# Optimization experiments

Hardware: AMD Instinct MI355X
Metric: run time of the kernel (lower is better)

The kernel has to match this reference:

```python
import jax, jax.numpy as jnp
import numpy as np

D_MODEL = 256
D_AUDIO = 256
W2V_DIM = 768
LIB_DIM = 93
N_LAYERS = 4
D_STATE = 16
D_CONV = 4
EXPAND = 2
D_INNER = EXPAND * D_MODEL  # 512
DT_RANK = (D_MODEL + 15) // 16  # 16
B, L = 8, 1024


def _silu(x):
    return x * jax.nn.sigmoid(x)


def _layernorm(x, g, b):
    mu = jnp.mean(x, axis=-1, keepdims=True)
    var = jnp.mean((x - mu) ** 2, axis=-1, keepdims=True)
    return (x - mu) * jax.lax.rsqrt(var + 1e-5) * g + b


def _mamba(x, in_W, conv_W, conv_b, xproj_W, dt_W, dt_b, A_log, D_vec, out_W):
    # x: [B, L, d_model]
    xz = jnp.einsum('bld,ed->ble', x, in_W)          # [B, L, 2*d_inner]
    xc, z = jnp.split(xz, 2, axis=-1)
    # causal depthwise conv1d over time
    u = jnp.swapaxes(xc, 1, 2)                        # [B, d_inner, L]
    u = jax.lax.conv_general_dilated(
        u, conv_W[:, None, :], (1,), [(D_CONV - 1, 0)],
        dimension_numbers=('NCH', 'OIH', 'NCH'), feature_group_count=D_INNER)
    xc = _silu(jnp.swapaxes(u, 1, 2) + conv_b)        # [B, L, d_inner]
    dbl = jnp.einsum('bld,ed->ble', xc, xproj_W)      # [B, L, dt_rank+2*d_state]
    dt, Bm, Cm = jnp.split(dbl, [DT_RANK, DT_RANK + D_STATE], axis=-1)
    dt = jax.nn.softplus(jnp.einsum('blr,dr->bld', dt, dt_W) + dt_b)  # [B, L, d_inner]
    A = -jnp.exp(A_log)                               # [d_inner, d_state]

    def step(h, inp):
        dt_t, x_t, B_t, C_t = inp                     # [B,d_inner],[B,d_inner],[B,S],[B,S]
        dA = jnp.exp(dt_t[..., None] * A)             # [B, d_inner, S]
        h = h * dA + (dt_t * x_t)[..., None] * B_t[:, None, :]
        y = jnp.einsum('bds,bs->bd', h, C_t)
        return h, y

    h0 = jnp.zeros((x.shape[0], D_INNER, D_STATE), x.dtype)
    xs = (jnp.swapaxes(dt, 0, 1), jnp.swapaxes(xc, 0, 1),
          jnp.swapaxes(Bm, 0, 1), jnp.swapaxes(Cm, 0, 1))
    _, ys = jax.lax.scan(step, h0, xs)                # ys: [L, B, d_inner]
    y = jnp.swapaxes(ys, 0, 1) + xc * D_vec
    y = y * _silu(z)
    return jnp.einsum('bld,ed->ble', y, out_W)


def setup_inputs() -> dict:
    key = jax.random.key(0)
    ks = jax.random.split(key, 24)

    def g(k, shape, scale):
        return (jax.random.normal(k, shape, dtype=jnp.float32) * scale)

    inp = {}
    inp['wav2vec_feat'] = jax.random.normal(ks[0], (B, L, W2V_DIM), dtype=jnp.float32)
    inp['librosa_feat'] = jax.random.normal(ks[1], (B, L, LIB_DIM), dtype=jnp.float32)
    inp['w2v_W'] = g(ks[2], (D_AUDIO, W2V_DIM), W2V_DIM ** -0.5)
    inp['w2v_b'] = jnp.zeros((D_AUDIO,), jnp.float32)
    inp['lib_W'] = g(ks[3], (D_AUDIO, LIB_DIM), LIB_DIM ** -0.5)
    inp['lib_b'] = jnp.zeros((D_AUDIO,), jnp.float32)
    inp['fuse_W'] = g(ks[4], (D_MODEL, 2 * D_AUDIO), (2 * D_AUDIO) ** -0.5)
    inp['fuse_b'] = jnp.zeros((D_MODEL,), jnp.float32)
    inp['proj_W'] = g(ks[5], (D_MODEL, D_MODEL), D_MODEL ** -0.5)
    inp['proj_b'] = jnp.zeros((D_MODEL,), jnp.float32)
    # stacked per-layer Mamba params, leading dim = N_LAYERS
    inp['ln_g'] = jnp.ones((N_LAYERS, D_MODEL), jnp.float32)
    inp['ln_b'] = jnp.zeros((N_LAYERS, D_MODEL), jnp.float32)
    inp['in_W'] = g(ks[6], (N_LAYERS, 2 * D_INNER, D_MODEL), D_MODEL ** -0.5)
    inp['conv_W'] = g(ks[7], (N_LAYERS, D_INNER, D_CONV), D_CONV ** -0.5)
    inp['conv_b'] = jnp.zeros((N_LAYERS, D_INNER), jnp.float32)
    inp['xproj_W'] = g(ks[8], (N_LAYERS, DT_RANK + 2 * D_STATE, D_INNER), D_INNER ** -0.5)
    inp['dt_W'] = g(ks[9], (N_LAYERS, D_INNER, DT_RANK), DT_RANK ** -0.5)
    inp['dt_b'] = jnp.full((N_LAYERS, D_INNER), -4.6, jnp.float32)  # softplus -> ~0.01
    A0 = jnp.log(jnp.arange(1, D_STATE + 1, dtype=jnp.float32))
    inp['A_log'] = jnp.broadcast_to(A0, (N_LAYERS, D_INNER, D_STATE)).copy()
    inp['D_vec'] = jnp.ones((N_LAYERS, D_INNER), jnp.float32)
    inp['out_W'] = g(ks[10], (N_LAYERS, D_MODEL, D_INNER), D_INNER ** -0.5)
    inp['fnorm_g'] = jnp.ones((D_MODEL,), jnp.float32)
    inp['fnorm_b'] = jnp.zeros((D_MODEL,), jnp.float32)
    return inp


def reference(wav2vec_feat, librosa_feat, w2v_W, w2v_b, lib_W, lib_b,
              fuse_W, fuse_b, proj_W, proj_b, ln_g, ln_b, in_W, conv_W, conv_b,
              xproj_W, dt_W, dt_b, A_log, D_vec, out_W, fnorm_g, fnorm_b):
    w = jnp.einsum('bld,ed->ble', wav2vec_feat, w2v_W) + w2v_b
    l = jnp.einsum('bld,ed->ble', librosa_feat, lib_W) + lib_b
    h = jnp.einsum('bld,ed->ble', jnp.concatenate([w, l], axis=-1), fuse_W) + fuse_b
    # MambaEncoder: proj -> blocks -> final norm
    h = jnp.einsum('bld,ed->ble', h, proj_W) + proj_b
    for i in range(N_LAYERS):
        h = h + _mamba(_layernorm(h, ln_g[i], ln_b[i]), in_W[i], conv_W[i],
                       conv_b[i], xproj_W[i], dt_W[i], dt_b[i], A_log[i],
                       D_vec[i], out_W[i])
    return _layernorm(h, fnorm_g, fnorm_b)
```

## Files before the change

### kernel.cpp

```cpp
#include <hip/hip_runtime.h>
#include <math.h>


#define CH 64
#define CT 16

typedef __attribute__((ext_vector_type(8))) short bfrag8;
typedef __attribute__((ext_vector_type(4))) float floatx4;

__device__ __forceinline__ float silu_f(float x) { return x / (1.f + __expf(-x)); }
__device__ __forceinline__ unsigned short f2bf(float x) {
    union { float f; unsigned int u; } c; c.f = x;
    unsigned int r = (c.u + 0x7fffu + ((c.u >> 16) & 1u)) >> 16;
    return (unsigned short)r;
}
__device__ __forceinline__ float bf2f(unsigned short u) {
    union { unsigned int u; float f; } c; c.u = ((unsigned int)u) << 16; return c.f;
}
__device__ __forceinline__ floatx4 exp4(floatx4 x) {
    floatx4 r;
    r[0] = __expf(x[0]); r[1] = __expf(x[1]); r[2] = __expf(x[2]); r[3] = __expf(x[3]);
    return r;
}

#define NJOBS 6
struct CvtJobs {
    const float* src[NJOBS];
    unsigned short* dst[NJOBS];
    int n_tot[NJOBS];
    int start_blk[NJOBS + 1];
};
__global__ void conv_bf16_multi(CvtJobs J)
{
    int blk = blockIdx.x;
    int job = 0;
    while (job + 1 < NJOBS && blk >= J.start_blk[job + 1]) job++;
    int i = (blk - J.start_blk[job]) * 1024 + threadIdx.x * 4;
    if (i >= J.n_tot[job]) return;
    const float* src = J.src[job];
    unsigned short* dst = J.dst[job];
    float4 v = *(const float4*)(src + i);
    dst[i] = f2bf(v.x); dst[i+1] = f2bf(v.y); dst[i+2] = f2bf(v.z); dst[i+3] = f2bf(v.w);
}

__global__ void pad_bf16_kernel(const float* __restrict__ src, unsigned short* __restrict__ dst,
                                int rows, int cs, int cd)
{
    int i = blockIdx.x * 256 + threadIdx.x;
    if (i >= rows * cd) return;
    int row = i / cd, c = i - row * cd;
    dst[i] = (c < cs) ? f2bf(src[row * cs + c]) : (unsigned short)0;
}

template<int RM, int RN>
__global__ __launch_bounds__(64)
void dmfma_gemm(const unsigned short* __restrict__ A, int lda,
                const unsigned short* __restrict__ W, int ldw,
                int K, const float* __restrict__ bias, const float* __restrict__ Cin,
                float* __restrict__ Cf32, unsigned short* __restrict__ Cbf16,
                int N, int ldc, int act)
{
    int lane = threadIdx.x;
    int lm = lane & 15, qk = lane >> 4;
    int m0 = blockIdx.y * (16 * RM);
    int n0 = blockIdx.x * (16 * RN);

    const unsigned short* Ab = A + (size_t)(m0 + lm) * lda + qk * 8;
    const unsigned short* Wb = W + (size_t)(n0 + lm) * ldw + qk * 8;

    floatx4 acc[RM][RN];
#pragma unroll
    for (int i = 0; i < RM; i++)
#pragma unroll
        for (int j = 0; j < RN; j++) acc[i][j] = (floatx4){0.f, 0.f, 0.f, 0.f};

    bfrag8 af[RM], wf[RN];
#pragma unroll
    for (int i = 0; i < RM; i++) af[i] = *(const bfrag8*)(Ab + (size_t)i * 16 * lda);
#pragma unroll
    for (int j = 0; j < RN; j++) wf[j] = *(const bfrag8*)(Wb + (size_t)j * 16 * ldw);

    for (int k0 = 32; k0 < K; k0 += 32) {
        bfrag8 afn[RM], wfn[RN];
#pragma unroll
        for (int i = 0; i < RM; i++) afn[i] = *(const bfrag8*)(Ab + (size_t)i * 16 * lda + k0);
#pragma unroll
        for (int j = 0; j < RN; j++) wfn[j] = *(const bfrag8*)(Wb + (size_t)j * 16 * ldw + k0);
#pragma unroll
        for (int i = 0; i < RM; i++)
#pragma unroll
            for (int j = 0; j < RN; j++)
                acc[i][j] = __builtin_amdgcn_mfma_f32_16x16x32_bf16(af[i], wf[j], acc[i][j], 0, 0, 0);
#pragma unroll
        for (int i = 0; i < RM; i++) af[i] = afn[i];
#pragma unroll
        for (int j = 0; j < RN; j++) wf[j] = wfn[j];
    }
#pragma unroll
    for (int i = 0; i < RM; i++)
#pragma unroll
        for (int j = 0; j < RN; j++)
            acc[i][j] = __builtin_amdgcn_mfma_f32_16x16x32_bf16(af[i], wf[j], acc[i][j], 0, 0, 0);

#pragma unroll
    for (int i = 0; i < RM; i++) {
        int mrow = m0 + i * 16 + qk * 4;
#pragma unroll
        for (int j = 0; j < RN; j++) {
            int n = n0 + j * 16 + lm;
            if (n < N) {
#pragma unroll
                for (int r = 0; r < 4; r++) {
                    float v = acc[i][j][r];
                    size_t o = (size_t)(mrow + r) * ldc + n;
                    if (bias) v += bias[n];
                    if (act == 1) v = fmaxf(v, 0.f) + log1pf(__expf(-fabsf(v)));
                    if (Cin) v += Cin[o];
                    if (Cf32) Cf32[o] = v;
                    if (Cbf16) Cbf16[o] = f2bf(v);
                }
            }
        }
    }
}

__global__ void ln_kernel(const float* __restrict__ x, const float* __restrict__ g,
                          const float* __restrict__ b, float* __restrict__ yf,
                          unsigned short* __restrict__ ybf)
{
    int row = blockIdx.x * 4 + (threadIdx.x >> 6);
    int lane = threadIdx.x & 63;
    size_t o = (size_t)row * 256 + lane * 4;
    floatx4 v = *(const floatx4*)(x + o);
    float s1 = v[0] + v[1] + v[2] + v[3];
    float s2 = v[0]*v[0] + v[1]*v[1] + v[2]*v[2] + v[3]*v[3];
#pragma unroll
    for (int off = 1; off < 64; off <<= 1) {
        s1 += __shfl_xor(s1, off);
        s2 += __shfl_xor(s2, off);
    }
    float mu = s1 * (1.f / 256.f);
    float var = s2 * (1.f / 256.f) - mu * mu;
    float rs = rsqrtf(var + 1e-5f);
    floatx4 gv = *(const floatx4*)(g + lane * 4);
    floatx4 bv = *(const floatx4*)(b + lane * 4);
    floatx4 out = (v - mu) * rs * gv + bv;
    if (yf) *(floatx4*)(yf + o) = out;
    if (ybf) {
        ushort4 pk;
        pk.x = f2bf(out[0]); pk.y = f2bf(out[1]); pk.z = f2bf(out[2]); pk.w = f2bf(out[3]);
        *(ushort4*)(ybf + o) = pk;
    }
}

__global__ void conv_silu_kernel(const unsigned short* __restrict__ xz, const float* __restrict__ cw,
                                 const float* __restrict__ cb, unsigned short* __restrict__ xc)
{
    int idx = blockIdx.x * 256 + threadIdx.x;
    int d4 = (idx & 127) << 2;
    int bt = idx >> 7;
    int t = bt & 1023;
    floatx4 acc = *(const floatx4*)(cb + d4);
    floatx4 w0 = *(const floatx4*)(cw + d4 * 4);
    floatx4 w1 = *(const floatx4*)(cw + d4 * 4 + 4);
    floatx4 w2 = *(const floatx4*)(cw + d4 * 4 + 8);
    floatx4 w3 = *(const floatx4*)(cw + d4 * 4 + 12);
#pragma unroll
    for (int j = 0; j < 4; j++) {
        int tt = t + j - 3;
        if (tt >= 0) {
            ushort4 v = *(const ushort4*)(xz + (size_t)(bt + j - 3) * 1024 + d4);
            acc[0] += bf2f(v.x) * w0[j];
            acc[1] += bf2f(v.y) * w1[j];
            acc[2] += bf2f(v.z) * w2[j];
            acc[3] += bf2f(v.w) * w3[j];
        }
    }
    ushort4 o;
    o.x = f2bf(silu_f(acc[0])); o.y = f2bf(silu_f(acc[1]));
    o.z = f2bf(silu_f(acc[2])); o.w = f2bf(silu_f(acc[3]));
    *(ushort4*)(xc + (size_t)bt * 512 + d4) = o;
}

__global__ __launch_bounds__(256, 4)
void scan_local_kernel(const unsigned short* __restrict__ xc, const float* __restrict__ dbl,
                       const unsigned short* __restrict__ dtb, const float* __restrict__ A_log,
                       const float* __restrict__ Dvec,
                       float* __restrict__ dtsums, float* __restrict__ Hbuf,
                       float* __restrict__ ypart)
{
    int bi = blockIdx.x;
    int dgrp = bi & 1;
    int chunk = (bi >> 1) & (CH - 1);
    int b = bi >> 7;
    int d = dgrp * 256 + threadIdx.x;

    floatx4 a0 = -exp4(*(const floatx4*)(A_log + d * 16));
    floatx4 a1 = -exp4(*(const floatx4*)(A_log + d * 16 + 4));
    floatx4 a2 = -exp4(*(const floatx4*)(A_log + d * 16 + 8));
    floatx4 a3 = -exp4(*(const floatx4*)(A_log + d * 16 + 12));
    float dcoef = Dvec[d];

    floatx4 z4 = (floatx4){0.f, 0.f, 0.f, 0.f};
    floatx4 h0 = z4, h1 = z4, h2 = z4, h3 = z4;
    float dtsum = 0.f;

    size_t rbt = (size_t)b * 1024 + chunk * CT;
    float dt_v = bf2f(dtb[rbt * 512 + d]);
    float x_v  = bf2f(xc[rbt * 512 + d]);
    const float* row = dbl + rbt * 48;
    floatx4 B0 = *(const floatx4*)(row + 16);
    floatx4 B1 = *(const floatx4*)(row + 20);
    floatx4 B2 = *(const floatx4*)(row + 24);
    floatx4 B3 = *(const floatx4*)(row + 28);

    for (int t = 0; t < CT - 1; t++) {
        size_t r2 = rbt + 1;
        float dt_n = bf2f(dtb[r2 * 512 + d]);
        float x_n  = bf2f(xc[r2 * 512 + d]);
        const float* rown = dbl + r2 * 48;
        floatx4 Bn0 = *(const floatx4*)(rown + 16);
        floatx4 Bn1 = *(const floatx4*)(rown + 20);
        floatx4 Bn2 = *(const floatx4*)(rown + 24);
        floatx4 Bn3 = *(const floatx4*)(rown + 28);

        float dtx = dt_v * x_v;
        dtsum += dt_v;
        floatx4 dA;
        dA = exp4(dt_v * a0); h0 = h0 * dA + dtx * B0;
        dA = exp4(dt_v * a1); h1 = h1 * dA + dtx * B1;
        dA = exp4(dt_v * a2); h2 = h2 * dA + dtx * B2;
        dA = exp4(dt_v * a3); h3 = h3 * dA + dtx * B3;
        floatx4 C0 = *(const floatx4*)(row + 32);
        floatx4 C1 = *(const floatx4*)(row + 36);
        floatx4 C2 = *(const floatx4*)(row + 40);
        floatx4 C3 = *(const floatx4*)(row + 44);
        floatx4 yv = h0 * C0 + h1 * C1 + h2 * C2 + h3 * C3;
        ypart[rbt * 512 + d] = yv[0] + yv[1] + yv[2] + yv[3] + x_v * dcoef;

        dt_v = dt_n; x_v = x_n;
        B0 = Bn0; B1 = Bn1; B2 = Bn2; B3 = Bn3;
        row = rown; rbt = r2;
    }
    {
        float dtx = dt_v * x_v;
        dtsum += dt_v;
        floatx4 dA;
        dA = exp4(dt_v * a0); h0 = h0 * dA + dtx * B0;
        dA = exp4(dt_v * a1); h1 = h1 * dA + dtx * B1;
        dA = exp4(dt_v * a2); h2 = h2 * dA + dtx * B2;
        dA = exp4(dt_v * a3); h3 = h3 * dA + dtx * B3;
        floatx4 C0 = *(const floatx4*)(row + 32);
        floatx4 C1 = *(const floatx4*)(row + 36);
        floatx4 C2 = *(const floatx4*)(row + 40);
        floatx4 C3 = *(const floatx4*)(row + 44);
        floatx4 yv = h0 * C0 + h1 * C1 + h2 * C2 + h3 * C3;
        ypart[rbt * 512 + d] = yv[0] + yv[1] + yv[2] + yv[3] + x_v * dcoef;
    }
    size_t base = (size_t)chunk * 65536 + ((b * 512 + d) * 16);
    *(floatx4*)&Hbuf[base]      = h0;
    *(floatx4*)&Hbuf[base + 4]  = h1;
    *(floatx4*)&Hbuf[base + 8]  = h2;
    *(floatx4*)&Hbuf[base + 12] = h3;
    dtsums[chunk * 4096 + b * 512 + d] = dtsum;
}

__global__ void scan_carry_kernel(const float* __restrict__ dtsums, const float* __restrict__ A_log,
                                  float* __restrict__ Hbuf)
{
    int ch = blockIdx.x * 256 + threadIdx.x;
    int s = ch & 15;
    int bd = ch >> 4;
    int d = bd & 511;
    float a = -__expf(A_log[d * 16 + s]);
    float h = 0.f;
#pragma unroll 8
    for (int c = 0; c < CH; c++) {
        float hl = Hbuf[(size_t)c * 65536 + ch];
        float P = __expf(dtsums[c * 4096 + bd] * a);
        Hbuf[(size_t)c * 65536 + ch] = h;
        h = fmaf(P, h, hl);
    }
}

__global__ __launch_bounds__(256, 4)
void scan_corr_kernel(const unsigned short* __restrict__ dtb, const float* __restrict__ dbl,
                      const unsigned short* __restrict__ xz, const float* __restrict__ ypart,
                      const float* __restrict__ A_log, const float* __restrict__ Hbuf,
                      unsigned short* __restrict__ y)
{
    int bi = blockIdx.x;
    int dgrp = bi & 1;
    int chunk = (bi >> 1) & (CH - 1);
    int b = bi >> 7;
    int d = dgrp * 256 + threadIdx.x;

    floatx4 a0 = -exp4(*(const floatx4*)(A_log + d * 16));
    floatx4 a1 = -exp4(*(const floatx4*)(A_log + d * 16 + 4));
    floatx4 a2 = -exp4(*(const floatx4*)(A_log + d * 16 + 8));
    floatx4 a3 = -exp4(*(const floatx4*)(A_log + d * 16 + 12));

    size_t base = (size_t)chunk * 65536 + ((b * 512 + d) * 16);
    floatx4 h0 = *(const floatx4*)&Hbuf[base];
    floatx4 h1 = *(const floatx4*)&Hbuf[base + 4];
    floatx4 h2 = *(const floatx4*)&Hbuf[base + 8];
    floatx4 h3 = *(const floatx4*)&Hbuf[base + 12];

    float S = 0.f;
    size_t rbt = (size_t)b * 1024 + chunk * CT;
#pragma unroll 4
    for (int t = 0; t < CT; t++, rbt++) {
        float dt_v = bf2f(dtb[rbt * 512 + d]);
        S += dt_v;
        const float* row = dbl + rbt * 48;
        floatx4 C0 = *(const floatx4*)(row + 32);
        floatx4 C1 = *(const floatx4*)(row + 36);
        floatx4 C2 = *(const floatx4*)(row + 40);
        floatx4 C3 = *(const floatx4*)(row + 44);
        floatx4 cv = (h0 * exp4(S * a0)) * C0 + (h1 * exp4(S * a1)) * C1
                   + (h2 * exp4(S * a2)) * C2 + (h3 * exp4(S * a3)) * C3;
        float corr = cv[0] + cv[1] + cv[2] + cv[3];
        float yp = ypart[rbt * 512 + d];
        float z  = bf2f(xz[rbt * 1024 + 512 + d]);
        y[rbt * 512 + d] = f2bf((yp + corr) * silu_f(z));
    }
}

extern "C" void kernel_launch(void* const* d_in, const int* in_sizes, int n_in,
                              void* d_out, int out_size, void* d_ws, size_t ws_size,
                              hipStream_t stream)
{
    const float* wav     = (const float*)d_in[0];
    const float* lib     = (const float*)d_in[1];
    const float* w2v_W   = (const float*)d_in[2];
    const float* w2v_b   = (const float*)d_in[3];
    const float* lib_W   = (const float*)d_in[4];
    const float* lib_b   = (const float*)d_in[5];
    const float* fuse_W  = (const float*)d_in[6];
    const float* fuse_b  = (const float*)d_in[7];
    const float* proj_W  = (const float*)d_in[8];
    const float* proj_b  = (const float*)d_in[9];
    const float* ln_g    = (const float*)d_in[10];
    const float* ln_b    = (const float*)d_in[11];
    const float* in_W    = (const float*)d_in[12];
    const float* conv_W  = (const float*)d_in[13];
    const float* conv_b  = (const float*)d_in[14];
    const float* xproj_W = (const float*)d_in[15];
    const float* dt_W    = (const float*)d_in[16];
    const float* dt_b    = (const float*)d_in[17];
    const float* A_log   = (const float*)d_in[18];
    const float* D_vec   = (const float*)d_in[19];
    const float* out_W   = (const float*)d_in[20];
    const float* fnorm_g = (const float*)d_in[21];
    const float* fnorm_b = (const float*)d_in[22];

    char* p = (char*)d_ws;
    float* hbuf = (float*)p;             p += 8192 * 256 * 4;
    unsigned short* xz_bf = (unsigned short*)p; p += (size_t)8192 * 1024 * 2;
    float* dblb = (float*)p;             p += 8192 * 48 * 4;
    unsigned short* dbl_bf = (unsigned short*)p; p += 8192 * 48 * 2;
    float* dtsums = (float*)p;           p += (size_t)CH * 4096 * 4;
    float* Hbuf = (float*)p;             p += (size_t)CH * 65536 * 4;
    float* ypart = (float*)p;            p += (size_t)8192 * 512 * 4;
    unsigned short* xln_bf = (unsigned short*)p; p += 8192 * 256 * 2;
    unsigned short* xcb_bf = (unsigned short*)p; p += 8192 * 512 * 2;
    unsigned short* dtb_bf = (unsigned short*)p; p += 8192 * 512 * 2;
    unsigned short* yb_bf  = (unsigned short*)p; p += 8192 * 512 * 2;
    unsigned short* w2vWb  = (unsigned short*)p; p += 256 * 768 * 2;
    unsigned short* fuseWb = (unsigned short*)p; p += 256 * 512 * 2;
    unsigned short* projWb = (unsigned short*)p; p += 256 * 256 * 2;
    unsigned short* inWb   = (unsigned short*)p; p += 4 * 1024 * 256 * 2;
    unsigned short* outWb  = (unsigned short*)p; p += 4 * 256 * 512 * 2;
    unsigned short* xprojWb= (unsigned short*)p; p += 4 * 64 * 512 * 2;
    unsigned short* dtWb   = (unsigned short*)p; p += 4 * 512 * 32 * 2;
    unsigned short* lib_bf = (unsigned short*)p; p += 8192 * 96 * 2;
    unsigned short* libWb  = (unsigned short*)p; p += 256 * 96 * 2;
    unsigned short* wav_bf  = xcb_bf;
    unsigned short* cat_bf  = yb_bf;
    unsigned short* fuse_bf = xln_bf;

    dim3 blk(256);
    dim3 wblk(64);

    CvtJobs J;
    const float* srcs[NJOBS] = { wav, w2v_W, fuse_W, proj_W, in_W, out_W };
    unsigned short* dsts[NJOBS] = { wav_bf, w2vWb, fuseWb, projWb, inWb, outWb };
    int ntot[NJOBS] = { 6291456, 196608, 131072, 65536, 1048576, 524288 };
    int sb = 0;
    for (int j = 0; j < NJOBS; j++) {
        J.src[j] = srcs[j]; J.dst[j] = dsts[j]; J.n_tot[j] = ntot[j];
        J.start_blk[j] = sb; sb += ntot[j] / 1024;
    }
    J.start_blk[NJOBS] = sb;
    conv_bf16_multi<<<sb, blk, 0, stream>>>(J);
    pad_bf16_kernel<<<(8192 * 96 + 255) / 256, blk, 0, stream>>>(lib, lib_bf, 8192, 93, 96);
    pad_bf16_kernel<<<(256 * 96 + 255) / 256, blk, 0, stream>>>(lib_W, libWb, 256, 93, 96);
    pad_bf16_kernel<<<(4 * 32768 + 255) / 256, blk, 0, stream>>>(xproj_W, xprojWb, 4, 24576, 32768);
    pad_bf16_kernel<<<(2048 * 32 + 255) / 256, blk, 0, stream>>>(dt_W, dtWb, 2048, 16, 32);

    dmfma_gemm<2,2><<<dim3(8, 256), wblk, 0, stream>>>(wav_bf, 768, w2vWb, 768, 768, w2v_b,
                                                       nullptr, nullptr, cat_bf, 256, 512, 0);
    dmfma_gemm<2,2><<<dim3(8, 256), wblk, 0, stream>>>(lib_bf, 96, libWb, 96, 96, lib_b,
                                                       nullptr, nullptr, cat_bf + 256, 256, 512, 0);
    dmfma_gemm<2,2><<<dim3(8, 256), wblk, 0, stream>>>(cat_bf, 512, fuseWb, 512, 512, fuse_b,
                                                       nullptr, nullptr, fuse_bf, 256, 256, 0);
    dmfma_gemm<2,2><<<dim3(8, 256), wblk, 0, stream>>>(fuse_bf, 256, projWb, 256, 256, proj_b,
                                                       nullptr, hbuf, nullptr, 256, 256, 0);

    for (int i = 0; i < 4; i++) {
        ln_kernel<<<2048, blk, 0, stream>>>(hbuf, ln_g + i * 256, ln_b + i * 256, nullptr, xln_bf);
        dmfma_gemm<2,4><<<dim3(16, 256), wblk, 0, stream>>>(xln_bf, 256, inWb + (size_t)i * 262144, 256,
                                                            256, nullptr, nullptr, nullptr, xz_bf, 1024, 1024, 0);
        conv_silu_kernel<<<4096, blk, 0, stream>>>(xz_bf, conv_W + i * 2048, conv_b + i * 512, xcb_bf);
        dmfma_gemm<1,2><<<dim3(2, 512), wblk, 0, stream>>>(xcb_bf, 512, xprojWb + (size_t)i * 32768, 512,
                                                           512, nullptr, nullptr, dblb, dbl_bf, 48, 48, 0);
        dmfma_gemm<2,4><<<dim3(8, 256), wblk, 0, stream>>>(dbl_bf, 48, dtWb + (size_t)i * 16384, 32,
                                                           32, dt_b + i * 512, nullptr, nullptr, dtb_bf, 512, 512, 1);
        scan_local_kernel<<<1024, blk, 0, stream>>>(xcb_bf, dblb, dtb_bf, A_log + i * 8192,
                                                    D_vec + i * 512, dtsums, Hbuf, ypart);
        scan_carry_kernel<<<256, blk, 0, stream>>>(dtsums, A_log + i * 8192, Hbuf);
        scan_corr_kernel<<<1024, blk, 0, stream>>>(dtb_bf, dblb, xz_bf, ypart,
                                                   A_log + i * 8192, Hbuf, yb_bf);
        dmfma_gemm<2,2><<<dim3(8, 256), wblk, 0, stream>>>(yb_bf, 512, outWb + (size_t)i * 131072, 512,
                                                           512, nullptr, hbuf, hbuf, nullptr, 256, 256, 0);
    }

    ln_kernel<<<2048, blk, 0, stream>>>(hbuf, fnorm_g, fnorm_b, (float*)d_out, nullptr);
}
```

Baseline: 771.6 us.

## Add LDS-tiled 4-wave MFMA GEMM for the dense projections

Adds a new bf16 MFMA GEMM that uses 256-thread blocks with 64x64 output tiles. Each K-step of 32 stages the A and W slices in shared memory, so all four waves reuse them. It replaces the single-wave, direct-from-global GEMM in the input-feature, fuse, proj, in_proj and out_proj matmuls. The aim is to cut redundant global loads and raise MFMA work per block. The tradeoff is two barriers per K-step and no double buffering of the shared tiles.

After: 668.1 us. 1.15x faster.

```diff
diff --git a/kernel.cpp b/kernel.cpp
--- a/kernel.cpp
+++ b/kernel.cpp
@@ -50,6 +50,82 @@
     if (i >= rows * cd) return;
     int row = i / cd, c = i - row * cd;
     dst[i] = (c < cs) ? f2bf(src[row * cs + c]) : (unsigned short)0;
+}
+
+template<int FR, int FC>
+__global__ __launch_bounds__(256)
+void smfma_gemm(const unsigned short* __restrict__ A, int lda,
+                const unsigned short* __restrict__ W, int ldw,
+                int K, const float* __restrict__ bias, const float* __restrict__ Cin,
+                float* __restrict__ Cf32, unsigned short* __restrict__ Cbf16,
+                int N, int ldc)
+{
+    const int BM = 2 * FR * 16, BN = 2 * FC * 16;
+    const int AR = BM / 64, WR2 = BN / 64;
+    __shared__ unsigned short lsA[BM * 40];
+    __shared__ unsigned short lsW[BN * 40];
+    int tid = threadIdx.x;
+    int lane = tid & 63, wave = tid >> 6;
+    int wr = wave >> 1, wc = wave & 1;
+    int qm = lane >> 4, lm = lane & 15;
+    int m0 = blockIdx.y * BM, n0 = blockIdx.x * BN;
+
+    int srow = tid >> 2;
+    int skoff = (tid & 3) * 8;
+    const unsigned short* Ag = A + (size_t)(m0 + srow) * lda + skoff;
+    const unsigned short* Wg = W + (size_t)(n0 + srow) * ldw + skoff;
+
+    floatx4 acc[FR][FC];
+#pragma unroll
+    for (int i = 0; i < FR; i++)
+#pragma unroll
+        for (int j = 0; j < FC; j++) acc[i][j] = (floatx4){0.f, 0.f, 0.f, 0.f};
+
+    for (int k0 = 0; k0 < K; k0 += 32) {
+        uint4 av[AR], wv[WR2];
+#pragma unroll
+        for (int r = 0; r < AR; r++)  av[r] = *(const uint4*)(Ag + (size_t)(r * 64) * lda + k0);
+#pragma unroll
+        for (int r = 0; r < WR2; r++) wv[r] = *(const uint4*)(Wg + (size_t)(r * 64) * ldw + k0);
+        __syncthreads();
+#pragma unroll
+        for (int r = 0; r < AR; r++)  *(uint4*)&lsA[(srow + r * 64) * 40 + skoff] = av[r];
+#pragma unroll
+        for (int r = 0; r < WR2; r++) *(uint4*)&lsW[(srow + r * 64) * 40 + skoff] = wv[r];
+        __syncthreads();
+        bfrag8 af[FR], wf[FC];
+#pragma unroll
+        for (int i = 0; i < FR; i++)
+            af[i] = *(bfrag8*)&lsA[(wr * FR * 16 + i * 16 + lm) * 40 + qm * 8];
+#pragma unroll
+        for (int j = 0; j < FC; j++)
+            wf[j] = *(bfrag8*)&lsW[(wc * FC * 16 + j * 16 + lm) * 40 + qm * 8];
+#pragma unroll
+        for (int i = 0; i < FR; i++)
+#pragma unroll
+            for (int j = 0; j < FC; j++)
+                acc[i][j] = __builtin_amdgcn_mfma_f32_16x16x32_bf16(af[i], wf[j], acc[i][j], 0, 0, 0);
+    }
+
+#pragma unroll
+    for (int i = 0; i < FR; i++) {
+        int mrow = m0 + wr * FR * 16 + i * 16 + qm * 4;
+#pragma unroll
+        for (int j = 0; j < FC; j++) {
+            int n = n0 + wc * FC * 16 + j * 16 + lm;
+            if (n < N) {
+#pragma unroll
+                for (int r = 0; r < 4; r++) {
+                    float v = acc[i][j][r];
+                    size_t o = (size_t)(mrow + r) * ldc + n;
+                    if (bias) v += bias[n];
+                    if (Cin) v += Cin[o];
+                    if (Cf32) Cf32[o] = v;
+                    if (Cbf16) Cbf16[o] = f2bf(v);
+                }
+            }
+        }
+    }
 }
 
 template<int RM, int RN>
@@ -398,19 +474,19 @@
     pad_bf16_kernel<<<(4 * 32768 + 255) / 256, blk, 0, stream>>>(xproj_W, xprojWb, 4, 24576, 32768);
     pad_bf16_kernel<<<(2048 * 32 + 255) / 256, blk, 0, stream>>>(dt_W, dtWb, 2048, 16, 32);
 
-    dmfma_gemm<2,2><<<dim3(8, 256), wblk, 0, stream>>>(wav_bf, 768, w2vWb, 768, 768, w2v_b,
-                                                       nullptr, nullptr, cat_bf, 256, 512, 0);
-    dmfma_gemm<2,2><<<dim3(8, 256), wblk, 0, stream>>>(lib_bf, 96, libWb, 96, 96, lib_b,
-                                                       nullptr, nullptr, cat_bf + 256, 256, 512, 0);
-    dmfma_gemm<2,2><<<dim3(8, 256), wblk, 0, stream>>>(cat_bf, 512, fuseWb, 512, 512, fuse_b,
-                                                       nullptr, nullptr, fuse_bf, 256, 256, 0);
-    dmfma_gemm<2,2><<<dim3(8, 256), wblk, 0, stream>>>(fuse_bf, 256, projWb, 256, 256, proj_b,
-                                                       nullptr, hbuf, nullptr, 256, 256, 0);
+    smfma_gemm<2,2><<<dim3(4, 128), blk, 0, stream>>>(wav_bf, 768, w2vWb, 768, 768, w2v_b,
+                                                      nullptr, nullptr, cat_bf, 256, 512);
+    smfma_gemm<2,2><<<dim3(4, 128), blk, 0, stream>>>(lib_bf, 96, libWb, 96, 96, lib_b,
+                                                      nullptr, nullptr, cat_bf + 256, 256, 512);
+    smfma_gemm<2,2><<<dim3(4, 128), blk, 0, stream>>>(cat_bf, 512, fuseWb, 512, 512, fuse_b,
+                                                      nullptr, nullptr, fuse_bf, 256, 256);
+    smfma_gemm<2,2><<<dim3(4, 128), blk, 0, stream>>>(fuse_bf, 256, projWb, 256, 256, proj_b,
+                                                      nullptr, hbuf, nullptr, 256, 256);
 
     for (int i = 0; i < 4; i++) {
         ln_kernel<<<2048, blk, 0, stream>>>(hbuf, ln_g + i * 256, ln_b + i * 256, nullptr, xln_bf);
-        dmfma_gemm<2,4><<<dim3(16, 256), wblk, 0, stream>>>(xln_bf, 256, inWb + (size_t)i * 262144, 256,
-                                                            256, nullptr, nullptr, nullptr, xz_bf, 1024, 1024, 0);
+        smfma_gemm<2,2><<<dim3(16, 128), blk, 0, stream>>>(xln_bf, 256, inWb + (size_t)i * 262144, 256,
+                                                           256, nullptr, nullptr, nullptr, xz_bf, 1024, 1024);
         conv_silu_kernel<<<4096, blk, 0, stream>>>(xz_bf, conv_W + i * 2048, conv_b + i * 512, xcb_bf);
         dmfma_gemm<1,2><<<dim3(2, 512), wblk, 0, stream>>>(xcb_bf, 512, xprojWb + (size_t)i * 32768, 512,
                                                            512, nullptr, nullptr, dblb, dbl_bf, 48, 48, 0);
@@ -421,8 +497,8 @@
         scan_carry_kernel<<<256, blk, 0, stream>>>(dtsums, A_log + i * 8192, Hbuf);
         scan_corr_kernel<<<1024, blk, 0, stream>>>(dtb_bf, dblb, xz_bf, ypart,
                                                    A_log + i * 8192, Hbuf, yb_bf);
-        dmfma_gemm<2,2><<<dim3(8, 256), wblk, 0, stream>>>(yb_bf, 512, outWb + (size_t)i * 131072, 512,
-                                                           512, nullptr, hbuf, hbuf, nullptr, 256, 256, 0);
+        smfma_gemm<2,2><<<dim3(4, 128), blk, 0, stream>>>(yb_bf, 512, outWb + (size_t)i * 131072, 512,
+                                                          512, nullptr, hbuf, hbuf, nullptr, 256, 256);
     }
 
     ln_kernel<<<2048, blk, 0, stream>>>(hbuf, fnorm_g, fnorm_b, (float*)d_out, nullptr);
```
